# Optimization experiments

Measured on AMD Instinct MI355X. Metric: run time of the kernel, lower is better.

The kernel has to match this reference:

```python
import jax, jax.numpy as jnp
import numpy as np
import math

D_MODEL = 1024
N_HEADS = 16
HEAD_DIM = D_MODEL // N_HEADS  # 64
B, T = 2, 2048


def _rotate_half(x):
    x1, x2 = jnp.split(x, 2, axis=-1)
    return jnp.concatenate([-x2, x1], axis=-1)


def _rope_sin_cos(seq_len, dim, dtype=jnp.float32):
    # matches RotaryEmbedding: inv_freq over even indices, emb = [freqs, freqs]
    inv_freq = 1.0 / (10000.0 ** (jnp.arange(0, dim, 2, dtype=dtype) / dim))
    t = jnp.arange(seq_len, dtype=dtype)
    freqs = jnp.einsum('i,j->ij', t, inv_freq)          # [T, dim/2]
    emb = jnp.concatenate((freqs, freqs), axis=-1)      # [T, dim]
    sin = jnp.sin(emb)[None, :, None, :]                # [1, T, 1, dim]
    cos = jnp.cos(emb)[None, :, None, :]
    return sin, cos


def setup_inputs() -> dict:
    key = jax.random.key(0)
    k1, k2, k3 = jax.random.split(key, 3)
    x = jax.random.normal(k1, (B, T, D_MODEL), dtype=jnp.float32)
    # causal mask broadcast over batch and heads: [1, 1, T, T]
    mask = jnp.tril(jnp.ones((T, T), dtype=bool))[None, None]
    w_qkv = jax.random.normal(k2, (D_MODEL, 3 * D_MODEL), dtype=jnp.float32) / math.sqrt(D_MODEL)
    w_out = jax.random.normal(k3, (D_MODEL, D_MODEL), dtype=jnp.float32) / math.sqrt(D_MODEL)
    return {"x": x, "mask": mask, "w_qkv": w_qkv, "w_out": w_out}


def reference(x, mask, w_qkv, w_out):
    Bx, Tx, Dx = x.shape
    qkv = x @ w_qkv                                     # [B, T, 3D]
    q, k, v = jnp.split(qkv, 3, axis=-1)
    q = q.reshape(Bx, Tx, N_HEADS, HEAD_DIM)
    k = k.reshape(Bx, Tx, N_HEADS, HEAD_DIM)
    v = v.reshape(Bx, Tx, N_HEADS, HEAD_DIM)
    sin, cos = _rope_sin_cos(Tx, HEAD_DIM, x.dtype)
    q = q * cos + _rotate_half(q) * sin
    k = k * cos + _rotate_half(k) * sin
    scores = jnp.einsum('bthd,bThd->bhtT', q, k) / math.sqrt(HEAD_DIM)
    scores = jnp.where(mask, scores, -1e10)
    probs = jax.nn.softmax(scores, axis=-1)             # [B, H, T, T]
    out = jnp.einsum('bhtT,bThd->bthd', probs, v)
    out = out.reshape(Bx, Tx, Dx)
    return out @ w_out
```

## Files before the change

### kernel.cpp

```cpp
#include <hip/hip_runtime.h>
#include <math.h>

typedef unsigned short u16;
typedef __attribute__((ext_vector_type(8))) short short8;
typedef __attribute__((ext_vector_type(4))) float f32x4;

__device__ __forceinline__ u16 f2bf(float f) {
  unsigned int u = __float_as_uint(f);
  u += 0x7fffu + ((u >> 16) & 1u);
  return (u16)(u >> 16);
}
__device__ __forceinline__ float bf2f(u16 h) {
  return __uint_as_float(((unsigned int)h) << 16);
}

__device__ __forceinline__ f32x4 mfma16(short8 a, short8 b, f32x4 c) {
  return __builtin_amdgcn_mfma_f32_16x16x32_bf16(a, b, c, 0, 0, 0);
}

#define NEG_BIG (-1e30f)

__global__ __launch_bounds__(256) void detect_dtype3(const u16* __restrict__ a,
                                                     const u16* __restrict__ bb,
                                                     const u16* __restrict__ c,
                                                     int* __restrict__ flags) {
  const u16* x = (blockIdx.x == 0) ? a : (blockIdx.x == 1) ? bb : c;
  __shared__ int cnt;
  if (threadIdx.x == 0) cnt = 0;
  __syncthreads();
  int my = 0;
  for (int i = threadIdx.x; i < 4096; i += 256) {
    float v = bf2f(x[2 * i]);
    float av = fabsf(v);
    if (v == 0.0f || (av >= 1e-4f && av <= 100.0f)) my++;
  }
  atomicAdd(&cnt, my);
  __syncthreads();
  if (threadIdx.x == 0) flags[blockIdx.x] = (cnt > 2458) ? 1 : 0;
}

__global__ __launch_bounds__(256) void prep_kernel(const void* __restrict__ wqkv,
                                                   const void* __restrict__ wout,
                                                   u16* __restrict__ wqkvT,
                                                   u16* __restrict__ woutT,
                                                   float2* __restrict__ tab,
                                                   const int* __restrict__ flags) {
  int z = blockIdx.z;
  int tid = threadIdx.x;
  if (z == 2) {
    if (blockIdx.x >= 16 || blockIdx.y >= 16) return;
    int idx = (blockIdx.y * 16 + blockIdx.x) * 256 + tid;
    int t = idx >> 5, d = idx & 31;
    float invf = expf(-(float)d * 0.28782313662425575f);
    float s, c;
    sincosf((float)t * invf, &s, &c);
    tab[idx] = make_float2(c, s);
    return;
  }
  const void* in = (z == 0) ? wqkv : wout;
  u16* out = (z == 0) ? wqkvT : woutT;
  int C = (z == 0) ? 3072 : 1024;
  const int R = 1024;
  bool isbf = (flags[z + 1] != 0);
  if (z == 1 && blockIdx.x >= 16) return;
  __shared__ float tile[64][68];
  int tc = blockIdx.x * 64, tr = blockIdx.y * 64;
  int r = tid >> 3, cg = (tid & 7) << 3;
#pragma unroll
  for (int p = 0; p < 2; ++p) {
    int row = r + p * 32;
    if (isbf) {
      short8 v = *(const short8*)((const u16*)in + (size_t)(tr + row) * C + tc + cg);
#pragma unroll
      for (int u = 0; u < 8; ++u) tile[row][cg + u] = bf2f((u16)v[u]);
    } else {
      const float* inf = (const float*)in + (size_t)(tr + row) * C + tc + cg;
#pragma unroll
      for (int u = 0; u < 8; ++u) tile[row][cg + u] = inf[u];
    }
  }
  __syncthreads();
#pragma unroll
  for (int p = 0; p < 2; ++p) {
    int orow = r + p * 32;
    short8 v;
#pragma unroll
    for (int u = 0; u < 8; ++u) v[u] = (short)f2bf(tile[cg + u][orow]);
    *(short8*)(out + (size_t)(tc + orow) * R + tr + cg) = v;
  }
}

__global__ __launch_bounds__(256) void convert_x(const void* __restrict__ xin,
                                                 u16* __restrict__ xb,
                                                 const int* __restrict__ flag) {
  bool isbf = (*flag != 0);
  int base = (blockIdx.x * 256 + threadIdx.x) * 8;
  if (isbf) {
    *(short8*)(xb + base) = *(const short8*)((const u16*)xin + base);
  } else {
    const float* xf = (const float*)xin;
    f32x4 x0 = *(const f32x4*)(xf + base);
    f32x4 x1 = *(const f32x4*)(xf + base + 4);
    short8 o;
#pragma unroll
    for (int u = 0; u < 4; ++u) { o[u] = (short)f2bf(x0[u]); o[u + 4] = (short)f2bf(x1[u]); }
    *(short8*)(xb + base) = o;
  }
}

__device__ __forceinline__ void qkv_epilogue2(f32x4 acc[4][4], int bm, int bn,
                                              int wm, int wn, int quad, int lane15,
                                              int lane, const float2* __restrict__ tab,
                                              u16* Qo, u16* Ko, u16* VTo, u16* eplds) {
  int nbase = bn + wn * 64;
  int h = (nbase & 1023) >> 6;
  bool isV = nbase >= 2048;
  if (!isV) {
#pragma unroll
    for (int i = 0; i < 4; ++i) {
#pragma unroll
      for (int r = 0; r < 4; ++r) {
        int mloc = i * 16 + quad * 4 + r;
        int t = (bm + wm * 64 + mloc) & 2047;
        float2 cs0 = tab[t * 32 + lane15];
        float2 cs1 = tab[t * 32 + 16 + lane15];
        float v0 = acc[i][0][r], v1 = acc[i][1][r], v2 = acc[i][2][r], v3 = acc[i][3][r];
        eplds[mloc * 68 + lane15]      = f2bf(v0 * cs0.x - v2 * cs0.y);
        eplds[mloc * 68 + 16 + lane15] = f2bf(v1 * cs1.x - v3 * cs1.y);
        eplds[mloc * 68 + 32 + lane15] = f2bf(v2 * cs0.x + v0 * cs0.y);
        eplds[mloc * 68 + 48 + lane15] = f2bf(v3 * cs1.x + v1 * cs1.y);
      }
    }
    asm volatile("s_waitcnt lgkmcnt(0)" ::: "memory");
    u16* dst = (nbase < 1024) ? Qo : Ko;
#pragma unroll
    for (int p = 0; p < 8; ++p) {
      int f = p * 64 + lane;
      int mr = f >> 3, nc = f & 7;
      int g = bm + wm * 64 + mr;
      int bI = g >> 11, tI = g & 2047;
      short8 val = *(const short8*)(eplds + mr * 68 + nc * 8);
      *(short8*)(dst + ((size_t)(bI * 16 + h) * 2048 + tI) * 64 + nc * 8) = val;
    }
  } else {
#pragma unroll
    for (int i = 0; i < 4; ++i)
#pragma unroll
      for (int j = 0; j < 4; ++j)
#pragma unroll
        for (int r = 0; r < 4; ++r)
          eplds[(j * 16 + lane15) * 68 + i * 16 + quad * 4 + r] = f2bf(acc[i][j][r]);
    asm volatile("s_waitcnt lgkmcnt(0)" ::: "memory");
    int g0 = bm + wm * 64;
    int bI = g0 >> 11, t0 = g0 & 2047;
#pragma unroll
    for (int p = 0; p < 8; ++p) {
      int f = p * 64 + lane;
      int dr = f >> 3, tc = f & 7;
      short8 val = *(const short8*)(eplds + dr * 68 + tc * 8);
      *(short8*)(VTo + ((size_t)(bI * 16 + h) * 64 + dr) * 2048 + t0 + tc * 8) = val;
    }
  }
}

__global__ __launch_bounds__(256) void gemm_qkv_fast(const u16* __restrict__ X,
                                                     const u16* __restrict__ WT,
                                                     const float2* __restrict__ tab,
                                                     u16* __restrict__ Qo,
                                                     u16* __restrict__ Ko,
                                                     u16* __restrict__ VTo) {
  const int K = 1024;
  __shared__ u16 buf[4 * 4352];
  u16* lA = buf;
  u16* lB = buf + 4096;
  int tid = threadIdx.x;
  int wave = tid >> 6, lane = tid & 63;
  int lane15 = lane & 15, quad = lane >> 4;
  int wm = wave >> 1, wn = wave & 1;
  int bm = blockIdx.x * 128, bn = blockIdx.y * 128;
  f32x4 acc[4][4] = {};
  for (int k0 = 0; k0 < K; k0 += 32) {
    __syncthreads();
#pragma unroll
    for (int p = 0; p < 2; ++p) {
      int g = p * 4 + wave;
      int f = g * 64 + lane;
      int row = f >> 2, cc = (f & 3) << 3;
      __builtin_amdgcn_global_load_lds(
          (const __attribute__((address_space(1))) unsigned int*)(X + (size_t)(bm + row) * K + k0 + cc),
          (__attribute__((address_space(3))) unsigned int*)(lA + g * 512), 16, 0, 0);
      __builtin_amdgcn_global_load_lds(
          (const __attribute__((address_space(1))) unsigned int*)(WT + (size_t)(bn + row) * K + k0 + cc),
          (__attribute__((address_space(3))) unsigned int*)(lB + g * 512), 16, 0, 0);
    }
    __syncthreads();
    short8 af[4], bf[4];
#pragma unroll
    for (int i = 0; i < 4; ++i)
      af[i] = *(const short8*)(lA + (wm * 64 + i * 16 + lane15) * 32 + quad * 8);
#pragma unroll
    for (int j = 0; j < 4; ++j)
      bf[j] = *(const short8*)(lB + (wn * 64 + j * 16 + lane15) * 32 + quad * 8);
#pragma unroll
    for (int i = 0; i < 4; ++i)
#pragma unroll
      for (int j = 0; j < 4; ++j)
        acc[i][j] = mfma16(af[i], bf[j], acc[i][j]);
  }
  __syncthreads();
  qkv_epilogue2(acc, bm, bn, wm, wn, quad, lane15, lane, tab, Qo, Ko, VTo,
                buf + wave * 4352);
}

__global__ __launch_bounds__(256) void gemm_qkv_rope(const void* __restrict__ Xv,
                                                     const u16* __restrict__ WT,
                                                     const float2* __restrict__ tab,
                                                     u16* __restrict__ Qo,
                                                     u16* __restrict__ Ko,
                                                     u16* __restrict__ VTo,
                                                     const int* __restrict__ flag) {
  const int K = 1024;
  __shared__ u16 buf[4 * 4352];
  u16* lA = buf;
  u16* lB = buf + 5120;
  bool isbf = (*flag != 0);
  int tid = threadIdx.x;
  int wave = tid >> 6, lane = tid & 63;
  int lane15 = lane & 15, quad = lane >> 4;
  int wm = wave >> 1, wn = wave & 1;
  int bm = blockIdx.x * 128, bn = blockIdx.y * 128;
  int sr = tid >> 2, scg = (tid & 3) << 3;
  f32x4 acc[4][4] = {};
  for (int k0 = 0; k0 < K; k0 += 32) {
    __syncthreads();
#pragma unroll
    for (int p = 0; p < 2; ++p) {
      int row = sr + p * 64;
      if (isbf) {
        *(short8*)(lA + row * 40 + scg) =
            *(const short8*)((const u16*)Xv + (size_t)(bm + row) * K + k0 + scg);
      } else {
        const float* xf = (const float*)Xv + (size_t)(bm + row) * K + k0 + scg;
        f32x4 x0 = *(const f32x4*)(xf);
        f32x4 x1 = *(const f32x4*)(xf + 4);
        short8 o;
#pragma unroll
        for (int u = 0; u < 4; ++u) { o[u] = (short)f2bf(x0[u]); o[u + 4] = (short)f2bf(x1[u]); }
        *(short8*)(lA + row * 40 + scg) = o;
      }
      *(short8*)(lB + row * 40 + scg) = *(const short8*)(WT + (size_t)(bn + row) * K + k0 + scg);
    }
    __syncthreads();
    short8 af[4], bf[4];
#pragma unroll
    for (int i = 0; i < 4; ++i)
      af[i] = *(const short8*)(lA + (wm * 64 + i * 16 + lane15) * 40 + quad * 8);
#pragma unroll
    for (int j = 0; j < 4; ++j)
      bf[j] = *(const short8*)(lB + (wn * 64 + j * 16 + lane15) * 40 + quad * 8);
#pragma unroll
    for (int i = 0; i < 4; ++i)
#pragma unroll
      for (int j = 0; j < 4; ++j)
        acc[i][j] = mfma16(af[i], bf[j], acc[i][j]);
  }
  __syncthreads();
  qkv_epilogue2(acc, bm, bn, wm, wn, quad, lane15, lane, tab, Qo, Ko, VTo,
                buf + wave * 4352);
}

__device__ __forceinline__ short8 lds_frag(const u16* buf, int row, int chunk) {
  int s = chunk ^ (row & 7);
  return *(const short8*)(buf + row * 64 + s * 8);
}

__device__ __forceinline__ void stage_tile(const u16* gK, const u16* gV,
                                           u16* lK, u16* lV, int wave, int lane) {
#pragma unroll
  for (int p = 0; p < 2; ++p) {
    int f = (p * 4 + wave) * 64 + lane;
    int r = f >> 3;
    int c = (f & 7) ^ (r & 7);
    __builtin_amdgcn_global_load_lds(
        (const __attribute__((address_space(1))) unsigned int*)(gK + (size_t)r * 64 + c * 8),
        (__attribute__((address_space(3))) unsigned int*)(lK + (p * 4 + wave) * 512),
        16, 0, 0);
    __builtin_amdgcn_global_load_lds(
        (const __attribute__((address_space(1))) unsigned int*)(gV + (size_t)r * 2048 + c * 8),
        (__attribute__((address_space(3))) unsigned int*)(lV + (p * 4 + wave) * 512),
        16, 0, 0);
  }
}

__global__ __launch_bounds__(256, 4) void attn_fused(const u16* __restrict__ Q,
                                                     const u16* __restrict__ K,
                                                     const u16* __restrict__ VT,
                                                     u16* __restrict__ Ao) {
  int bx = blockIdx.x;
  int bh = bx & 31;
  int kp = bx >> 5;
  int m = kp & 7, n = kp >> 3;
  int qt = (n == 0) ? m : (n == 1) ? (15 - m) : (n == 2) ? (16 + m) : (31 - m);
  int b = bh >> 4, h = bh & 15;
  int tid = threadIdx.x, wave = tid >> 6, lane = tid & 63;
  int lane15 = lane & 15, quad = lane >> 4;
  int q0 = qt * 64 + wave * 16;
  const u16* Qb = Q + (size_t)bh * 2048 * 64;
  const u16* Kb = K + (size_t)bh * 2048 * 64;
  const u16* Vb = VT + (size_t)bh * 64 * 2048;

  __shared__ u16 Kl[2][64 * 64];
  __shared__ u16 Vl[2][64 * 64];
  __shared__ u16 lP[4][16 * 64];
  u16* myP = lP[wave];

  short8 qf0 = *(const short8*)(Qb + (size_t)(q0 + lane15) * 64 + quad * 8);
  short8 qf1 = *(const short8*)(Qb + (size_t)(q0 + lane15) * 64 + 32 + quad * 8);

  f32x4 Ov[4] = {};
  float tsum[4] = {0.f, 0.f, 0.f, 0.f};

  int ntiles = qt + 1;
  stage_tile(Kb, Vb, Kl[0], Vl[0], wave, lane);

  for (int kt = 0; kt < ntiles; ++kt) {
    int kbase = kt * 64;
    int cur = kt & 1;
    __syncthreads();
    if (kt + 1 < ntiles)
      stage_tile(Kb + (size_t)(kbase + 64) * 64, Vb + kbase + 64,
                 Kl[cur ^ 1], Vl[cur ^ 1], wave, lane);

    f32x4 S[4];
#pragma unroll
    for (int j = 0; j < 4; ++j) {
      short8 k0 = lds_frag(Kl[cur], j * 16 + lane15, quad);
      short8 k1 = lds_frag(Kl[cur], j * 16 + lane15, 4 + quad);
      f32x4 z = {};
      z = mfma16(qf0, k0, z);
      z = mfma16(qf1, k1, z);
      S[j] = z;
    }
    if (kt == qt) {
#pragma unroll
      for (int j = 0; j < 4; ++j) {
        int kpos = kbase + j * 16 + lane15;
#pragma unroll
        for (int r = 0; r < 4; ++r)
          if (kpos > q0 + quad * 4 + r) S[j][r] = NEG_BIG;
      }
    }
#pragma unroll
    for (int j = 0; j < 4; ++j)
#pragma unroll
      for (int r = 0; r < 4; ++r) {
        float p = __expf(fmaf(S[j][r], 0.125f, -8.0f));
        S[j][r] = p;
        tsum[r] += p;
      }
#pragma unroll
    for (int j = 0; j < 4; ++j)
#pragma unroll
      for (int r = 0; r < 4; ++r) {
        int lrow = quad * 4 + r;
        int slot = (j * 2 + (lane15 >> 3)) ^ (lrow & 7);
        myP[lrow * 64 + slot * 8 + (lane15 & 7)] = f2bf(S[j][r]);
      }
    asm volatile("s_waitcnt lgkmcnt(0)" ::: "memory");
    short8 pa0 = *(const short8*)(myP + lane15 * 64 + ((quad) ^ (lane15 & 7)) * 8);
    short8 pa1 = *(const short8*)(myP + lane15 * 64 + ((4 + quad) ^ (lane15 & 7)) * 8);
#pragma unroll
    for (int j = 0; j < 4; ++j) {
      short8 v0 = lds_frag(Vl[cur], j * 16 + lane15, quad);
      short8 v1 = lds_frag(Vl[cur], j * 16 + lane15, 4 + quad);
      Ov[j] = mfma16(pa0, v0, Ov[j]);
      Ov[j] = mfma16(pa1, v1, Ov[j]);
    }
  }
  float rl[4];
#pragma unroll
  for (int r = 0; r < 4; ++r) {
    float v = tsum[r];
    v += __shfl_xor(v, 1);
    v += __shfl_xor(v, 2);
    v += __shfl_xor(v, 4);
    v += __shfl_xor(v, 8);
    rl[r] = 1.f / v;
  }
#pragma unroll
  for (int j = 0; j < 4; ++j)
#pragma unroll
    for (int r = 0; r < 4; ++r) {
      int t = q0 + quad * 4 + r;
      Ao[(size_t)(b * 2048 + t) * 1024 + h * 64 + j * 16 + lane15] =
          f2bf(Ov[j][r] * rl[r]);
    }
}

__global__ __launch_bounds__(256) void gemm_out(const u16* __restrict__ A,
                                                const u16* __restrict__ WT,
                                                float* __restrict__ out) {
  const int K = 1024;
  __shared__ u16 lA[64 * 32];
  __shared__ u16 lB[128 * 32];
  int tid = threadIdx.x;
  int wave = tid >> 6, lane = tid & 63;
  int lane15 = lane & 15, quad = lane >> 4;
  int wm = wave >> 1, wn = wave & 1;
  int bm = blockIdx.x * 64, bn = blockIdx.y * 128;
  f32x4 acc[2][4] = {};
  for (int k0 = 0; k0 < K; k0 += 32) {
    __syncthreads();
#pragma unroll
    for (int q = 0; q < 3; ++q) {
      int blk = wave * 3 + q;
      int f, row, cc;
      if (blk < 4) {
        f = blk * 64 + lane;
        row = f >> 2;
        cc = (f & 3) << 3;
        __builtin_amdgcn_global_load_lds(
            (const __attribute__((address_space(1))) unsigned int*)(A + (size_t)(bm + row) * K + k0 + cc),
            (__attribute__((address_space(3))) unsigned int*)(lA + blk * 512), 16, 0, 0);
      } else {
        int bblk = blk - 4;
        f = bblk * 64 + lane;
        row = f >> 2;
        cc = (f & 3) << 3;
        __builtin_amdgcn_global_load_lds(
            (const __attribute__((address_space(1))) unsigned int*)(WT + (size_t)(bn + row) * K + k0 + cc),
            (__attribute__((address_space(3))) unsigned int*)(lB + bblk * 512), 16, 0, 0);
      }
    }
    __syncthreads();
    short8 af[2], bf[4];
#pragma unroll
    for (int i = 0; i < 2; ++i)
      af[i] = *(const short8*)(lA + (wm * 32 + i * 16 + lane15) * 32 + quad * 8);
#pragma unroll
    for (int j = 0; j < 4; ++j)
      bf[j] = *(const short8*)(lB + (wn * 64 + j * 16 + lane15) * 32 + quad * 8);
#pragma unroll
    for (int i = 0; i < 2; ++i)
#pragma unroll
      for (int j = 0; j < 4; ++j)
        acc[i][j] = mfma16(af[i], bf[j], acc[i][j]);
  }
#pragma unroll
  for (int i = 0; i < 2; ++i)
#pragma unroll
    for (int r = 0; r < 4; ++r) {
      int m = bm + wm * 32 + i * 16 + quad * 4 + r;
      size_t rowo = (size_t)m * 1024 + bn + wn * 64 + lane15;
      out[rowo] = acc[i][0][r];
      out[rowo + 16] = acc[i][1][r];
      out[rowo + 32] = acc[i][2][r];
      out[rowo + 48] = acc[i][3][r];
    }
}

__global__ void ws_sentinel(float* out, float val) {
  if (threadIdx.x == 0) out[1] = val;
}

extern "C" void kernel_launch(void* const* d_in, const int* in_sizes, int n_in,
                              void* d_out, int out_size, void* d_ws, size_t ws_size,
                              hipStream_t stream) {
  (void)out_size;
  const void* x = nullptr;
  const void* w_qkv = nullptr;
  const void* w_out = nullptr;
  for (int i = 0; i < n_in; ++i) {
    if (in_sizes[i] == 4194304 && !x) x = d_in[i];
    else if (in_sizes[i] == 3145728 && !w_qkv) w_qkv = d_in[i];
    else if (in_sizes[i] == 1048576 && !w_out) w_out = d_in[i];
  }
  float* out = (float*)d_out;

  const size_t EL_B = 32 + 4194304 + 1048576 + 3 * 4194304 + 262144;
  const size_t REQ_B = EL_B * 2;
  const size_t REQ_A = (EL_B + 4194304) * 2;
  if (ws_size < REQ_B) {
    ws_sentinel<<<1, 64, 0, stream>>>(out, 1.0e6f + 1000.0f * (float)(ws_size >> 20));
    return;
  }
  int* flags = (int*)d_ws;
  u16* base = (u16*)d_ws + 32;
  u16* wqkvT = base;
  u16* attnw = base;
  u16* woutT = base + 4194304;
  u16* Qw = woutT + 1048576;
  u16* Kw = Qw + 4194304;
  u16* VTw = Kw + 4194304;
  float2* tab = (float2*)(VTw + 4194304);
  u16* xb = VTw + 4194304 + 262144;

  detect_dtype3<<<3, 256, 0, stream>>>((const u16*)x, (const u16*)w_qkv,
                                       (const u16*)w_out, flags);
  prep_kernel<<<dim3(48, 16, 3), 256, 0, stream>>>(w_qkv, w_out, wqkvT, woutT, tab, flags);
  if (ws_size >= REQ_A) {
    convert_x<<<2048, 256, 0, stream>>>(x, xb, flags + 0);
    gemm_qkv_fast<<<dim3(32, 24), 256, 0, stream>>>(xb, wqkvT, tab, Qw, Kw, VTw);
  } else {
    gemm_qkv_rope<<<dim3(32, 24), 256, 0, stream>>>(x, wqkvT, tab, Qw, Kw, VTw, flags + 0);
  }
  attn_fused<<<1024, 256, 0, stream>>>(Qw, Kw, VTw, attnw);
  gemm_out<<<dim3(64, 8), 256, 0, stream>>>(attnw, woutT, out);
}
```

Measured before the change: 207.5 us.

## Widen GEMM K-tiles with XOR-swizzled LDS and fuse x conversion into prep

```diff
diff --git a/kernel.cpp b/kernel.cpp
--- a/kernel.cpp
+++ b/kernel.cpp
@@ -19,6 +19,12 @@
 }
 
 #define NEG_BIG (-1e30f)
+
+__device__ __forceinline__ void glds16(const u16* g, u16* l) {
+  __builtin_amdgcn_global_load_lds(
+      (const __attribute__((address_space(1))) unsigned int*)g,
+      (__attribute__((address_space(3))) unsigned int*)l, 16, 0, 0);
+}
 
 __global__ __launch_bounds__(256) void detect_dtype3(const u16* __restrict__ a,
                                                      const u16* __restrict__ bb,
@@ -39,12 +45,14 @@
   if (threadIdx.x == 0) flags[blockIdx.x] = (cnt > 2458) ? 1 : 0;
 }
 
-__global__ __launch_bounds__(256) void prep_kernel(const void* __restrict__ wqkv,
-                                                   const void* __restrict__ wout,
-                                                   u16* __restrict__ wqkvT,
-                                                   u16* __restrict__ woutT,
-                                                   float2* __restrict__ tab,
-                                                   const int* __restrict__ flags) {
+__global__ __launch_bounds__(256) void prep_all(const void* __restrict__ wqkv,
+                                                const void* __restrict__ wout,
+                                                const void* __restrict__ xin,
+                                                u16* __restrict__ wqkvT,
+                                                u16* __restrict__ woutT,
+                                                u16* __restrict__ xb,
+                                                float2* __restrict__ tab,
+                                                const int* __restrict__ flags) {
   int z = blockIdx.z;
   int tid = threadIdx.x;
   if (z == 2) {
@@ -57,6 +65,25 @@
     tab[idx] = make_float2(c, s);
     return;
   }
+  if (z == 3) {
+    bool isbf = (flags[0] != 0);
+    int tg = (blockIdx.y * 48 + blockIdx.x) * 256 + tid;
+    for (int i = tg; i < 524288; i += 196608) {
+      int base = i * 8;
+      if (isbf) {
+        *(short8*)(xb + base) = *(const short8*)((const u16*)xin + base);
+      } else {
+        const float* xf = (const float*)xin;
+        f32x4 x0 = *(const f32x4*)(xf + base);
+        f32x4 x1 = *(const f32x4*)(xf + base + 4);
+        short8 o;
+#pragma unroll
+        for (int u = 0; u < 4; ++u) { o[u] = (short)f2bf(x0[u]); o[u + 4] = (short)f2bf(x1[u]); }
+        *(short8*)(xb + base) = o;
+      }
+    }
+    return;
+  }
   const void* in = (z == 0) ? wqkv : wout;
   u16* out = (z == 0) ? wqkvT : woutT;
   int C = (z == 0) ? 3072 : 1024;
@@ -90,32 +117,14 @@
   }
 }
 
-__global__ __launch_bounds__(256) void convert_x(const void* __restrict__ xin,
-                                                 u16* __restrict__ xb,
-                                                 const int* __restrict__ flag) {
-  bool isbf = (*flag != 0);
-  int base = (blockIdx.x * 256 + threadIdx.x) * 8;
-  if (isbf) {
-    *(short8*)(xb + base) = *(const short8*)((const u16*)xin + base);
-  } else {
-    const float* xf = (const float*)xin;
-    f32x4 x0 = *(const f32x4*)(xf + base);
-    f32x4 x1 = *(const f32x4*)(xf + base + 4);
-    short8 o;
-#pragma unroll
-    for (int u = 0; u < 4; ++u) { o[u] = (short)f2bf(x0[u]); o[u + 4] = (short)f2bf(x1[u]); }
-    *(short8*)(xb + base) = o;
-  }
-}
-
-__device__ __forceinline__ void qkv_epilogue2(f32x4 acc[4][4], int bm, int bn,
+__device__ __forceinline__ void qkv_epilogue3(f32x4 acc[4][4], int bm, int bn,
                                               int wm, int wn, int quad, int lane15,
                                               int lane, const float2* __restrict__ tab,
-                                              u16* Qo, u16* Ko, u16* VTo, u16* eplds) {
+                                              u16* Qo, u16* Ko, u16* VTo, u16* myE) {
   int nbase = bn + wn * 64;
   int h = (nbase & 1023) >> 6;
-  bool isV = nbase >= 2048;
-  if (!isV) {
+  if (nbase < 2048) {
+    int l8 = lane15 & 7, lh = lane15 >> 3;
 #pragma unroll
     for (int i = 0; i < 4; ++i) {
 #pragma unroll
@@ -125,10 +134,12 @@
         float2 cs0 = tab[t * 32 + lane15];
         float2 cs1 = tab[t * 32 + 16 + lane15];
         float v0 = acc[i][0][r], v1 = acc[i][1][r], v2 = acc[i][2][r], v3 = acc[i][3][r];
-        eplds[mloc * 68 + lane15]      = f2bf(v0 * cs0.x - v2 * cs0.y);
-        eplds[mloc * 68 + 16 + lane15] = f2bf(v1 * cs1.x - v3 * cs1.y);
-        eplds[mloc * 68 + 32 + lane15] = f2bf(v2 * cs0.x + v0 * cs0.y);
-        eplds[mloc * 68 + 48 + lane15] = f2bf(v3 * cs1.x + v1 * cs1.y);
+        int m7 = mloc & 7;
+        u16* rowp = myE + mloc * 64 + l8;
+        rowp[((0 + lh) ^ m7) * 8] = f2bf(v0 * cs0.x - v2 * cs0.y);
+        rowp[((2 + lh) ^ m7) * 8] = f2bf(v1 * cs1.x - v3 * cs1.y);
+        rowp[((4 + lh) ^ m7) * 8] = f2bf(v2 * cs0.x + v0 * cs0.y);
+        rowp[((6 + lh) ^ m7) * 8] = f2bf(v3 * cs1.x + v1 * cs1.y);
       }
     }
     asm volatile("s_waitcnt lgkmcnt(0)" ::: "memory");
@@ -137,9 +148,9 @@
     for (int p = 0; p < 8; ++p) {
       int f = p * 64 + lane;
       int mr = f >> 3, nc = f & 7;
+      short8 val = *(const short8*)(myE + mr * 64 + (nc ^ (mr & 7)) * 8);
       int g = bm + wm * 64 + mr;
       int bI = g >> 11, tI = g & 2047;
-      short8 val = *(const short8*)(eplds + mr * 68 + nc * 8);
       *(short8*)(dst + ((size_t)(bI * 16 + h) * 2048 + tI) * 64 + nc * 8) = val;
     }
   } else {
@@ -148,8 +159,11 @@
 #pragma unroll
       for (int j = 0; j < 4; ++j)
 #pragma unroll
-        for (int r = 0; r < 4; ++r)
-          eplds[(j * 16 + lane15) * 68 + i * 16 + quad * 4 + r] = f2bf(acc[i][j][r]);
+        for (int r = 0; r < 4; ++r) {
+          int col = i * 16 + quad * 4 + r;
+          int slot = (col >> 3) ^ (lane15 & 7);
+          myE[(j * 16 + lane15) * 64 + slot * 8 + (col & 7)] = f2bf(acc[i][j][r]);
+        }
     asm volatile("s_waitcnt lgkmcnt(0)" ::: "memory");
     int g0 = bm + wm * 64;
     int bI = g0 >> 11, t0 = g0 & 2047;
@@ -157,7 +171,7 @@
     for (int p = 0; p < 8; ++p) {
       int f = p * 64 + lane;
       int dr = f >> 3, tc = f & 7;
-      short8 val = *(const short8*)(eplds + dr * 68 + tc * 8);
+      short8 val = *(const short8*)(myE + dr * 64 + (tc ^ (dr & 7)) * 8);
       *(short8*)(VTo + ((size_t)(bI * 16 + h) * 64 + dr) * 2048 + t0 + tc * 8) = val;
     }
   }
@@ -170,46 +184,47 @@
                                                      u16* __restrict__ Ko,
                                                      u16* __restrict__ VTo) {
   const int K = 1024;
-  __shared__ u16 buf[4 * 4352];
+  __shared__ u16 buf[16384];
   u16* lA = buf;
-  u16* lB = buf + 4096;
+  u16* lB = buf + 8192;
   int tid = threadIdx.x;
   int wave = tid >> 6, lane = tid & 63;
   int lane15 = lane & 15, quad = lane >> 4;
   int wm = wave >> 1, wn = wave & 1;
   int bm = blockIdx.x * 128, bn = blockIdx.y * 128;
   f32x4 acc[4][4] = {};
-  for (int k0 = 0; k0 < K; k0 += 32) {
-    __syncthreads();
-#pragma unroll
-    for (int p = 0; p < 2; ++p) {
+  for (int k0 = 0; k0 < K; k0 += 64) {
+    __syncthreads();
+#pragma unroll
+    for (int p = 0; p < 4; ++p) {
       int g = p * 4 + wave;
       int f = g * 64 + lane;
-      int row = f >> 2, cc = (f & 3) << 3;
-      __builtin_amdgcn_global_load_lds(
-          (const __attribute__((address_space(1))) unsigned int*)(X + (size_t)(bm + row) * K + k0 + cc),
-          (__attribute__((address_space(3))) unsigned int*)(lA + g * 512), 16, 0, 0);
-      __builtin_amdgcn_global_load_lds(
-          (const __attribute__((address_space(1))) unsigned int*)(WT + (size_t)(bn + row) * K + k0 + cc),
-          (__attribute__((address_space(3))) unsigned int*)(lB + g * 512), 16, 0, 0);
-    }
-    __syncthreads();
-    short8 af[4], bf[4];
-#pragma unroll
-    for (int i = 0; i < 4; ++i)
-      af[i] = *(const short8*)(lA + (wm * 64 + i * 16 + lane15) * 32 + quad * 8);
-#pragma unroll
-    for (int j = 0; j < 4; ++j)
-      bf[j] = *(const short8*)(lB + (wn * 64 + j * 16 + lane15) * 32 + quad * 8);
-#pragma unroll
-    for (int i = 0; i < 4; ++i)
+      int r = f >> 3;
+      int c8 = (f & 7) ^ (r & 7);
+      glds16(X + (size_t)(bm + r) * K + k0 + c8 * 8, lA + g * 512);
+      glds16(WT + (size_t)(bn + r) * K + k0 + c8 * 8, lB + g * 512);
+    }
+    __syncthreads();
+#pragma unroll
+    for (int ks = 0; ks < 2; ++ks) {
+      int so = ((ks * 4 + quad) ^ (lane15 & 7)) * 8;
+      short8 af[4], bf[4];
+#pragma unroll
+      for (int i = 0; i < 4; ++i)
+        af[i] = *(const short8*)(lA + (wm * 64 + i * 16 + lane15) * 64 + so);
 #pragma unroll
       for (int j = 0; j < 4; ++j)
-        acc[i][j] = mfma16(af[i], bf[j], acc[i][j]);
+        bf[j] = *(const short8*)(lB + (wn * 64 + j * 16 + lane15) * 64 + so);
+#pragma unroll
+      for (int i = 0; i < 4; ++i)
+#pragma unroll
+        for (int j = 0; j < 4; ++j)
+          acc[i][j] = mfma16(af[i], bf[j], acc[i][j]);
+    }
   }
   __syncthreads();
-  qkv_epilogue2(acc, bm, bn, wm, wn, quad, lane15, lane, tab, Qo, Ko, VTo,
-                buf + wave * 4352);
+  qkv_epilogue3(acc, bm, bn, wm, wn, quad, lane15, lane, tab, Qo, Ko, VTo,
+                buf + wave * 4096);
 }
 
 __global__ __launch_bounds__(256) void gemm_qkv_rope(const void* __restrict__ Xv,
@@ -220,7 +235,7 @@
                                                      u16* __restrict__ VTo,
                                                      const int* __restrict__ flag) {
   const int K = 1024;
-  __shared__ u16 buf[4 * 4352];
+  __shared__ u16 buf[16384];
   u16* lA = buf;
   u16* lB = buf + 5120;
   bool isbf = (*flag != 0);
@@ -265,8 +280,8 @@
         acc[i][j] = mfma16(af[i], bf[j], acc[i][j]);
   }
   __syncthreads();
-  qkv_epilogue2(acc, bm, bn, wm, wn, quad, lane15, lane, tab, Qo, Ko, VTo,
-                buf + wave * 4352);
+  qkv_epilogue3(acc, bm, bn, wm, wn, quad, lane15, lane, tab, Qo, Ko, VTo,
+                buf + wave * 4096);
 }
 
 __device__ __forceinline__ short8 lds_frag(const u16* buf, int row, int chunk) {
@@ -281,14 +296,8 @@
     int f = (p * 4 + wave) * 64 + lane;
     int r = f >> 3;
     int c = (f & 7) ^ (r & 7);
-    __builtin_amdgcn_global_load_lds(
-        (const __attribute__((address_space(1))) unsigned int*)(gK + (size_t)r * 64 + c * 8),
-        (__attribute__((address_space(3))) unsigned int*)(lK + (p * 4 + wave) * 512),
-        16, 0, 0);
-    __builtin_amdgcn_global_load_lds(
-        (const __attribute__((address_space(1))) unsigned int*)(gV + (size_t)r * 2048 + c * 8),
-        (__attribute__((address_space(3))) unsigned int*)(lV + (p * 4 + wave) * 512),
-        16, 0, 0);
+    glds16(gK + (size_t)r * 64 + c * 8, lK + (p * 4 + wave) * 512);
+    glds16(gV + (size_t)r * 2048 + c * 8, lV + (p * 4 + wave) * 512);
   }
 }
 
@@ -401,50 +410,49 @@
                                                 const u16* __restrict__ WT,
                                                 float* __restrict__ out) {
   const int K = 1024;
-  __shared__ u16 lA[64 * 32];
-  __shared__ u16 lB[128 * 32];
+  __shared__ u16 lA[64 * 128];
+  __shared__ u16 lB[128 * 128];
   int tid = threadIdx.x;
   int wave = tid >> 6, lane = tid & 63;
   int lane15 = lane & 15, quad = lane >> 4;
   int wm = wave >> 1, wn = wave & 1;
   int bm = blockIdx.x * 64, bn = blockIdx.y * 128;
   f32x4 acc[2][4] = {};
-  for (int k0 = 0; k0 < K; k0 += 32) {
-    __syncthreads();
-#pragma unroll
-    for (int q = 0; q < 3; ++q) {
-      int blk = wave * 3 + q;
-      int f, row, cc;
-      if (blk < 4) {
-        f = blk * 64 + lane;
-        row = f >> 2;
-        cc = (f & 3) << 3;
-        __builtin_amdgcn_global_load_lds(
-            (const __attribute__((address_space(1))) unsigned int*)(A + (size_t)(bm + row) * K + k0 + cc),
-            (__attribute__((address_space(3))) unsigned int*)(lA + blk * 512), 16, 0, 0);
-      } else {
-        int bblk = blk - 4;
-        f = bblk * 64 + lane;
-        row = f >> 2;
-        cc = (f & 3) << 3;
-        __builtin_amdgcn_global_load_lds(
-            (const __attribute__((address_space(1))) unsigned int*)(WT + (size_t)(bn + row) * K + k0 + cc),
-            (__attribute__((address_space(3))) unsigned int*)(lB + bblk * 512), 16, 0, 0);
-      }
-    }
-    __syncthreads();
-    short8 af[2], bf[4];
-#pragma unroll
-    for (int i = 0; i < 2; ++i)
-      af[i] = *(const short8*)(lA + (wm * 32 + i * 16 + lane15) * 32 + quad * 8);
-#pragma unroll
-    for (int j = 0; j < 4; ++j)
-      bf[j] = *(const short8*)(lB + (wn * 64 + j * 16 + lane15) * 32 + quad * 8);
-#pragma unroll
-    for (int i = 0; i < 2; ++i)
+  for (int k0 = 0; k0 < K; k0 += 128) {
+    __syncthreads();
+#pragma unroll
+    for (int p = 0; p < 4; ++p) {
+      int g = p * 4 + wave;
+      int f = g * 64 + lane;
+      int r = f >> 4;
+      int c16 = (f & 15) ^ (r & 15);
+      glds16(A + (size_t)(bm + r) * K + k0 + c16 * 8, lA + g * 512);
+    }
+#pragma unroll
+    for (int p = 0; p < 8; ++p) {
+      int g = p * 4 + wave;
+      int f = g * 64 + lane;
+      int r = f >> 4;
+      int c16 = (f & 15) ^ (r & 15);
+      glds16(WT + (size_t)(bn + r) * K + k0 + c16 * 8, lB + g * 512);
+    }
+    __syncthreads();
+#pragma unroll
+    for (int ks = 0; ks < 4; ++ks) {
+      int so = ((ks * 4 + quad) ^ lane15) * 8;
+      short8 af[2], bf[4];
+#pragma unroll
+      for (int i = 0; i < 2; ++i)
+        af[i] = *(const short8*)(lA + (wm * 32 + i * 16 + lane15) * 128 + so);
 #pragma unroll
       for (int j = 0; j < 4; ++j)
-        acc[i][j] = mfma16(af[i], bf[j], acc[i][j]);
+        bf[j] = *(const short8*)(lB + (wn * 64 + j * 16 + lane15) * 128 + so);
+#pragma unroll
+      for (int i = 0; i < 2; ++i)
+#pragma unroll
+        for (int j = 0; j < 4; ++j)
+          acc[i][j] = mfma16(af[i], bf[j], acc[i][j]);
+    }
   }
 #pragma unroll
   for (int i = 0; i < 2; ++i)
@@ -497,11 +505,13 @@
 
   detect_dtype3<<<3, 256, 0, stream>>>((const u16*)x, (const u16*)w_qkv,
                                        (const u16*)w_out, flags);
-  prep_kernel<<<dim3(48, 16, 3), 256, 0, stream>>>(w_qkv, w_out, wqkvT, woutT, tab, flags);
   if (ws_size >= REQ_A) {
-    convert_x<<<2048, 256, 0, stream>>>(x, xb, flags + 0);
+    prep_all<<<dim3(48, 16, 4), 256, 0, stream>>>(w_qkv, w_out, x, wqkvT, woutT,
+                                                  xb, tab, flags);
     gemm_qkv_fast<<<dim3(32, 24), 256, 0, stream>>>(xb, wqkvT, tab, Qw, Kw, VTw);
   } else {
+    prep_all<<<dim3(48, 16, 3), 256, 0, stream>>>(w_qkv, w_out, x, wqkvT, woutT,
+                                                  nullptr, tab, flags);
     gemm_qkv_rope<<<dim3(32, 24), 256, 0, stream>>>(x, wqkvT, tab, Qw, Kw, VTw, flags + 0);
   }
   attn_fused<<<1024, 256, 0, stream>>>(Qw, Kw, VTw, attnw);
```

Result: no change. 204.6 us (-1.4%).
